# Performance work log

Hardware: AMD Instinct MI355X
Metric: run time of the kernel (lower is better)

The kernel has to match this reference:

```python
import jax, jax.numpy as jnp
import numpy as np

N_ATOMS = 1000
BOX_L = 30.0      # cubic cell edge (Angstrom)
MAX_CUTOFF = 8.0  # max(cutoff)


def _np_cart(a, b, c):
    # numpy equivalent of torch.cartesian_prod for 3 1-D arrays
    g = np.meshgrid(a, b, c, indexing='ij')
    return np.stack(g, axis=-1).reshape(-1, 3)


def _np_get_shifts(cell, cutoff):
    # mirrors TorchNeighborListRangeSeparated._get_shifts (pbc=True on all axes)
    recip = np.linalg.inv(cell).T
    inv_len = np.linalg.norm(recip, axis=1)
    nrep = np.ceil(cutoff * inv_len).astype(np.int64)
    r1 = np.arange(1, nrep[0] + 1, dtype=np.float64)
    r2 = np.arange(1, nrep[1] + 1, dtype=np.float64)
    r3 = np.arange(1, nrep[2] + 1, dtype=np.float64)
    o = np.zeros(1, dtype=np.float64)
    return np.concatenate([
        _np_cart(r1, r2, r3), _np_cart(r1, r2, o), _np_cart(r1, r2, -r3),
        _np_cart(r1, o, r3), _np_cart(r1, o, o), _np_cart(r1, o, -r3),
        _np_cart(r1, -r2, r3), _np_cart(r1, -r2, o), _np_cart(r1, -r2, -r3),
        _np_cart(o, r2, r3), _np_cart(o, r2, o), _np_cart(o, r2, -r3),
        _np_cart(o, o, r3)], axis=0)


def setup_inputs() -> dict:
    key = jax.random.key(0)
    cell_np = np.eye(3) * BOX_L
    shifts = jnp.asarray(_np_get_shifts(cell_np, MAX_CUTOFF), dtype=jnp.float32)  # [13,3]
    positions = jax.random.uniform(key, (N_ATOMS, 3), dtype=jnp.float32) * BOX_L
    return {
        "positions": positions,
        "cell": jnp.asarray(cell_np, dtype=jnp.float32),
        "shifts": shifts,
        "cutoffs": jnp.array([4.0, 8.0], dtype=jnp.float32),
    }


def reference(positions, cell, shifts, cutoffs):
    """PBC-aware pairwise distance^2 + per-cutoff neighbor masks.

    Returns:
      d2:    [P] squared distances over all candidate pairs
             (N*(N-1)/2 in-cell pairs followed by S*N*N shifted-image pairs)
      masks: [n_cutoffs, P] int32 in-cutoff indicator (d2 < cutoff^2)
    """
    n = positions.shape[0]
    # in-cell pairs (torch.combinations -> i<j)
    iu, ju = jnp.triu_indices(n, k=1)
    rij_c = positions[iu] - positions[ju]                       # [Pc,3]
    d2_c = jnp.sum(rij_c * rij_c, axis=-1)                      # [Pc]
    # shifted-image pairs: all (shift, i, j)
    shift_values = shifts @ cell                                # [S,3]
    rij_o = (positions[None, :, None, :] - positions[None, None, :, :]
             + shift_values[:, None, None, :])                  # [S,N,N,3]
    d2_o = jnp.sum(rij_o * rij_o, axis=-1).reshape(-1)          # [S*N*N]
    d2 = jnp.concatenate([d2_c, d2_o], axis=0)                  # [P]
    masks = (d2[None, :] < (cutoffs ** 2)[:, None]).astype(jnp.int32)
    return d2, masks
```

## Files before the change

### kernel.cpp

```cpp
#include <hip/hip_runtime.h>
#include <math.h>


__global__ void __launch_bounds__(256) nbr_kernel(
    const float* __restrict__ pos,
    const float* __restrict__ cell,
    const float* __restrict__ shifts,
    const float* __restrict__ cutoffs,
    int ncut, int n,
    float* __restrict__ out, long long P, long long Pc)
{
    long long p0 = ((long long)blockIdx.x * 256 + threadIdx.x) << 2;
    if (p0 >= P) return;

    double cut2[4];
    for (int c = 0; c < ncut; ++c) { double cv = (double)cutoffs[c]; cut2[c] = cv * cv; }

    float d2f[4];
    float mf[4][4];

    if (p0 >= Pc) {
        long long q = p0 - Pc;
        unsigned nn = (unsigned)n * (unsigned)n;
        unsigned s  = (unsigned)((unsigned long long)q / nn);
        unsigned r  = (unsigned)((unsigned long long)q - (unsigned long long)s * nn);
        unsigned i  = r / (unsigned)n;
        unsigned j0 = r - i * (unsigned)n;

        double s0 = (double)shifts[3*s+0], s1 = (double)shifts[3*s+1], s2 = (double)shifts[3*s+2];
        double sv0 = s0 * (double)cell[0] + s1 * (double)cell[3] + s2 * (double)cell[6];
        double sv1 = s0 * (double)cell[1] + s1 * (double)cell[4] + s2 * (double)cell[7];
        double sv2 = s0 * (double)cell[2] + s1 * (double)cell[5] + s2 * (double)cell[8];

        double pix = (double)pos[3*i+0];
        double piy = (double)pos[3*i+1];
        double piz = (double)pos[3*i+2];

        const float4* pj = (const float4*)(pos + 3 * j0);
        float4 a = pj[0], b = pj[1], c4 = pj[2];
        float jx[4] = {a.x, a.w, b.z, c4.y};
        float jy[4] = {a.y, b.x, b.w, c4.z};
        float jz[4] = {a.z, b.y, c4.x, c4.w};

        for (int k = 0; k < 4; ++k) {
            double dx = (pix - (double)jx[k]) + sv0;
            double dy = (piy - (double)jy[k]) + sv1;
            double dz = (piz - (double)jz[k]) + sv2;
            double d2 = dx*dx + dy*dy + dz*dz;
            d2f[k] = (float)d2;
            for (int c = 0; c < ncut; ++c) mf[c][k] = (d2 < cut2[c]) ? 1.0f : 0.0f;
        }
    } else {
        long long tn = 2LL * n - 1;
        for (int k = 0; k < 4; ++k) {
            long long p = p0 + k;
            double D = (double)(tn * tn) - 8.0 * (double)p;
            long long i = (long long)(((double)tn - sqrt(D)) * 0.5);
            if (i < 0) i = 0;
            if (i > n - 2) i = n - 2;
            while ((i + 1) * (tn - (i + 1)) / 2 <= p) ++i;
            while (i * (tn - i) / 2 > p) --i;
            long long j = p - i * (tn - i) / 2 + i + 1;

            double dx = (double)pos[3*i+0] - (double)pos[3*j+0];
            double dy = (double)pos[3*i+1] - (double)pos[3*j+1];
            double dz = (double)pos[3*i+2] - (double)pos[3*j+2];
            double d2 = dx*dx + dy*dy + dz*dz;
            d2f[k] = (float)d2;
            for (int c = 0; c < ncut; ++c) mf[c][k] = (d2 < cut2[c]) ? 1.0f : 0.0f;
        }
    }

    *(float4*)(out + p0) = make_float4(d2f[0], d2f[1], d2f[2], d2f[3]);
    for (int c = 0; c < ncut; ++c)
        *(float4*)(out + (long long)(c + 1) * P + p0) =
            make_float4(mf[c][0], mf[c][1], mf[c][2], mf[c][3]);
}

__global__ void __launch_bounds__(256) nbr_kernel_scalar(
    const float* __restrict__ pos,
    const float* __restrict__ cell,
    const float* __restrict__ shifts,
    const float* __restrict__ cutoffs,
    int ncut, int n,
    float* __restrict__ out, long long P, long long Pc)
{
    long long p = (long long)blockIdx.x * 256 + threadIdx.x;
    if (p >= P) return;

    double cut2[4];
    for (int c = 0; c < ncut; ++c) { double cv = (double)cutoffs[c]; cut2[c] = cv * cv; }

    double d2;
    if (p >= Pc) {
        long long q = p - Pc;
        unsigned long long nn = (unsigned long long)n * n;
        unsigned s = (unsigned)(q / nn);
        unsigned long long r = q - (unsigned long long)s * nn;
        unsigned i = (unsigned)(r / n);
        unsigned j = (unsigned)(r - (unsigned long long)i * n);
        double s0 = (double)shifts[3*s+0], s1 = (double)shifts[3*s+1], s2 = (double)shifts[3*s+2];
        double sv0 = s0*(double)cell[0] + s1*(double)cell[3] + s2*(double)cell[6];
        double sv1 = s0*(double)cell[1] + s1*(double)cell[4] + s2*(double)cell[7];
        double sv2 = s0*(double)cell[2] + s1*(double)cell[5] + s2*(double)cell[8];
        double dx = ((double)pos[3*i+0] - (double)pos[3*j+0]) + sv0;
        double dy = ((double)pos[3*i+1] - (double)pos[3*j+1]) + sv1;
        double dz = ((double)pos[3*i+2] - (double)pos[3*j+2]) + sv2;
        d2 = dx*dx + dy*dy + dz*dz;
    } else {
        long long tn = 2LL * n - 1;
        double D = (double)(tn * tn) - 8.0 * (double)p;
        long long i = (long long)(((double)tn - sqrt(D)) * 0.5);
        if (i < 0) i = 0;
        if (i > n - 2) i = n - 2;
        while ((i + 1) * (tn - (i + 1)) / 2 <= p) ++i;
        while (i * (tn - i) / 2 > p) --i;
        long long j = p - i * (tn - i) / 2 + i + 1;
        double dx = (double)pos[3*i+0] - (double)pos[3*j+0];
        double dy = (double)pos[3*i+1] - (double)pos[3*j+1];
        double dz = (double)pos[3*i+2] - (double)pos[3*j+2];
        d2 = dx*dx + dy*dy + dz*dz;
    }
    out[p] = (float)d2;
    for (int c = 0; c < ncut; ++c)
        out[(long long)(c + 1) * P + p] = (d2 < cut2[c]) ? 1.0f : 0.0f;
}

extern "C" void kernel_launch(void* const* d_in, const int* in_sizes, int n_in,
                              void* d_out, int out_size, void* d_ws, size_t ws_size,
                              hipStream_t stream)
{
    const float* pos     = (const float*)d_in[0];
    const float* cell    = (const float*)d_in[1];
    const float* shifts  = (const float*)d_in[2];
    const float* cutoffs = (const float*)d_in[3];
    int n    = in_sizes[0] / 3;
    int S    = in_sizes[2] / 3;
    int ncut = in_sizes[3];

    long long Pc = (long long)n * (n - 1) / 2;
    long long P  = Pc + (long long)S * n * n;
    float* out = (float*)d_out;

    if ((n & 3) == 0) {
        long long chunks = P >> 2;
        int blocks = (int)((chunks + 255) / 256);
        nbr_kernel<<<blocks, 256, 0, stream>>>(pos, cell, shifts, cutoffs,
                                               ncut, n, out, P, Pc);
    } else {
        int blocks = (int)((P + 255) / 256);
        nbr_kernel_scalar<<<blocks, 256, 0, stream>>>(pos, cell, shifts, cutoffs,
                                                      ncut, n, out, P, Pc);
    }
}
```

Before: 170.9 us.

## Map shifted pairs to a 3D grid, template cutoff count, use nontemporal stores

```diff
diff --git a/kernel.cpp b/kernel.cpp
--- a/kernel.cpp
+++ b/kernel.cpp
@@ -2,36 +2,36 @@
 #include <math.h>
 
 
-__global__ void __launch_bounds__(256) nbr_kernel(
+typedef float f32x4 __attribute__((ext_vector_type(4)));
+
+template <int NCUT>
+__global__ void __launch_bounds__(256) nbr_fast(
     const float* __restrict__ pos,
     const float* __restrict__ cell,
     const float* __restrict__ shifts,
     const float* __restrict__ cutoffs,
-    int ncut, int n,
-    float* __restrict__ out, long long P, long long Pc)
+    int n, int S,
+    float* __restrict__ out, unsigned P, unsigned Pc)
 {
-    long long p0 = ((long long)blockIdx.x * 256 + threadIdx.x) << 2;
-    if (p0 >= P) return;
+    const int tid = threadIdx.x;
+    const int s   = blockIdx.z;
 
-    double cut2[4];
-    for (int c = 0; c < ncut; ++c) { double cv = (double)cutoffs[c]; cut2[c] = cv * cv; }
+    double cut2[NCUT];
+#pragma unroll
+    for (int c = 0; c < NCUT; ++c) {
+        double cv = (double)cutoffs[c];
+        cut2[c] = cv * cv;
+    }
 
-    float d2f[4];
-    float mf[4][4];
-
-    if (p0 >= Pc) {
-        long long q = p0 - Pc;
-        unsigned nn = (unsigned)n * (unsigned)n;
-        unsigned s  = (unsigned)((unsigned long long)q / nn);
-        unsigned r  = (unsigned)((unsigned long long)q - (unsigned long long)s * nn);
-        unsigned i  = r / (unsigned)n;
-        unsigned j0 = r - i * (unsigned)n;
+    if (s < S) {
+        const unsigned j0 = (unsigned)tid << 2;
+        if (j0 >= (unsigned)n) return;
+        const unsigned i = blockIdx.y;
 
         double s0 = (double)shifts[3*s+0], s1 = (double)shifts[3*s+1], s2 = (double)shifts[3*s+2];
         double sv0 = s0 * (double)cell[0] + s1 * (double)cell[3] + s2 * (double)cell[6];
         double sv1 = s0 * (double)cell[1] + s1 * (double)cell[4] + s2 * (double)cell[7];
         double sv2 = s0 * (double)cell[2] + s1 * (double)cell[5] + s2 * (double)cell[8];
-
         double pix = (double)pos[3*i+0];
         double piy = (double)pos[3*i+1];
         double piz = (double)pos[3*i+2];
@@ -42,18 +42,34 @@
         float jy[4] = {a.y, b.x, b.w, c4.z};
         float jz[4] = {a.z, b.y, c4.x, c4.w};
 
+        f32x4 d2v;
+        f32x4 mv[NCUT];
+#pragma unroll
         for (int k = 0; k < 4; ++k) {
             double dx = (pix - (double)jx[k]) + sv0;
             double dy = (piy - (double)jy[k]) + sv1;
             double dz = (piz - (double)jz[k]) + sv2;
             double d2 = dx*dx + dy*dy + dz*dz;
-            d2f[k] = (float)d2;
-            for (int c = 0; c < ncut; ++c) mf[c][k] = (d2 < cut2[c]) ? 1.0f : 0.0f;
+            d2v[k] = (float)d2;
+#pragma unroll
+            for (int c = 0; c < NCUT; ++c) mv[c][k] = (d2 < cut2[c]) ? 1.0f : 0.0f;
         }
+
+        const unsigned t0 = ((unsigned)s * (unsigned)n + i) * (unsigned)n + j0 + Pc;
+        __builtin_nontemporal_store(d2v, (f32x4*)(out + t0));
+#pragma unroll
+        for (int c = 0; c < NCUT; ++c)
+            __builtin_nontemporal_store(mv[c], (f32x4*)(out + (unsigned)(c + 1) * P + t0));
     } else {
-        long long tn = 2LL * n - 1;
+        const unsigned p0 = ((blockIdx.y * 256u) + (unsigned)tid) << 2;
+        if (p0 >= Pc) return;
+
+        const long long tn = 2LL * n - 1;
+        f32x4 d2v;
+        f32x4 mv[NCUT];
+#pragma unroll
         for (int k = 0; k < 4; ++k) {
-            long long p = p0 + k;
+            long long p = (long long)p0 + k;
             double D = (double)(tn * tn) - 8.0 * (double)p;
             long long i = (long long)(((double)tn - sqrt(D)) * 0.5);
             if (i < 0) i = 0;
@@ -66,18 +82,19 @@
             double dy = (double)pos[3*i+1] - (double)pos[3*j+1];
             double dz = (double)pos[3*i+2] - (double)pos[3*j+2];
             double d2 = dx*dx + dy*dy + dz*dz;
-            d2f[k] = (float)d2;
-            for (int c = 0; c < ncut; ++c) mf[c][k] = (d2 < cut2[c]) ? 1.0f : 0.0f;
+            d2v[k] = (float)d2;
+#pragma unroll
+            for (int c = 0; c < NCUT; ++c) mv[c][k] = (d2 < cut2[c]) ? 1.0f : 0.0f;
         }
+
+        __builtin_nontemporal_store(d2v, (f32x4*)(out + p0));
+#pragma unroll
+        for (int c = 0; c < NCUT; ++c)
+            __builtin_nontemporal_store(mv[c], (f32x4*)(out + (unsigned)(c + 1) * P + p0));
     }
-
-    *(float4*)(out + p0) = make_float4(d2f[0], d2f[1], d2f[2], d2f[3]);
-    for (int c = 0; c < ncut; ++c)
-        *(float4*)(out + (long long)(c + 1) * P + p0) =
-            make_float4(mf[c][0], mf[c][1], mf[c][2], mf[c][3]);
 }
 
-__global__ void __launch_bounds__(256) nbr_kernel_scalar(
+__global__ void __launch_bounds__(256) nbr_scalar(
     const float* __restrict__ pos,
     const float* __restrict__ cell,
     const float* __restrict__ shifts,
@@ -87,9 +104,6 @@
 {
     long long p = (long long)blockIdx.x * 256 + threadIdx.x;
     if (p >= P) return;
-
-    double cut2[4];
-    for (int c = 0; c < ncut; ++c) { double cv = (double)cutoffs[c]; cut2[c] = cv * cv; }
 
     double d2;
     if (p >= Pc) {
@@ -122,8 +136,10 @@
         d2 = dx*dx + dy*dy + dz*dz;
     }
     out[p] = (float)d2;
-    for (int c = 0; c < ncut; ++c)
-        out[(long long)(c + 1) * P + p] = (d2 < cut2[c]) ? 1.0f : 0.0f;
+    for (int c = 0; c < ncut; ++c) {
+        double cv = (double)cutoffs[c];
+        out[(long long)(c + 1) * P + p] = (d2 < cv * cv) ? 1.0f : 0.0f;
+    }
 }
 
 extern "C" void kernel_launch(void* const* d_in, const int* in_sizes, int n_in,
@@ -142,14 +158,20 @@
     long long P  = Pc + (long long)S * n * n;
     float* out = (float*)d_out;
 
-    if ((n & 3) == 0) {
-        long long chunks = P >> 2;
-        int blocks = (int)((chunks + 255) / 256);
-        nbr_kernel<<<blocks, 256, 0, stream>>>(pos, cell, shifts, cutoffs,
-                                               ncut, n, out, P, Pc);
+    bool fast = ((n & 3) == 0) && (n <= 2049) && (ncut >= 1) && (ncut <= 4) &&
+                (3 * P < (1LL << 31));
+    if (fast) {
+        dim3 grid(1, n, S + 1);
+        unsigned uP = (unsigned)P, uPc = (unsigned)Pc;
+        switch (ncut) {
+        case 1: nbr_fast<1><<<grid, 256, 0, stream>>>(pos, cell, shifts, cutoffs, n, S, out, uP, uPc); break;
+        case 2: nbr_fast<2><<<grid, 256, 0, stream>>>(pos, cell, shifts, cutoffs, n, S, out, uP, uPc); break;
+        case 3: nbr_fast<3><<<grid, 256, 0, stream>>>(pos, cell, shifts, cutoffs, n, S, out, uP, uPc); break;
+        default: nbr_fast<4><<<grid, 256, 0, stream>>>(pos, cell, shifts, cutoffs, n, S, out, uP, uPc); break;
+        }
     } else {
         int blocks = (int)((P + 255) / 256);
-        nbr_kernel_scalar<<<blocks, 256, 0, stream>>>(pos, cell, shifts, cutoffs,
-                                                      ncut, n, out, P, Pc);
+        nbr_scalar<<<blocks, 256, 0, stream>>>(pos, cell, shifts, cutoffs,
+                                               ncut, n, out, P, Pc);
     }
 }
```

New measurement: 183.7 us. 1.07x slower.
